# Kernel tuning notes

Hardware: AMD Instinct MI355X
Metric: run time of the kernel (lower is better)

## Reference

```python
import jax, jax.numpy as jnp
import numpy as np

D_MODEL = 1024
N_HEADS = 16
FACTOR = 2
KEY_DIM = D_MODEL // N_HEADS            # 64
HEAD_DIM = D_MODEL * FACTOR // N_HEADS  # 128
SCALING = KEY_DIM ** -0.5
BSZ, SEQ = 2, 2048


def _rel_pos(slen):
    # angle: 1/10000**linspace(0,1,key_dim//2), each value repeated twice
    half = jnp.asarray(1.0) / jnp.power(10000.0, jnp.linspace(0.0, 1.0, KEY_DIM // 2))
    angle = jnp.repeat(half, 2)                              # [key_dim]
    decay = jnp.log(1.0 - 2.0 ** (-5.0 - jnp.arange(N_HEADS, dtype=jnp.float32)))  # [h], negative
    idx = jnp.arange(slen, dtype=jnp.float32)
    sin = jnp.sin(idx[:, None] * angle[None, :])             # [s, key_dim]
    cos = jnp.cos(idx[:, None] * angle[None, :])
    diff = idx[:, None] - idx[None, :]                       # [s, s]
    tril = diff >= 0
    mask = jnp.where(tril[None], jnp.exp(diff[None] * decay[:, None, None]), 0.0)  # [h, s, s]
    mask = mask / jnp.sqrt(mask.sum(axis=-1, keepdims=True))
    return sin, cos, mask


def _rotate_every_two(x):
    x1 = x[..., ::2]
    x2 = x[..., 1::2]
    return jnp.stack((-x2, x1), axis=-1).reshape(x.shape)


def _theta_shift(x, sin, cos):
    return x * cos + _rotate_every_two(x) * sin


def setup_inputs() -> dict:
    key = jax.random.key(0)
    ks = jax.random.split(key, 11)
    s = 1.0 / np.sqrt(D_MODEL)
    s2 = 1.0 / np.sqrt(D_MODEL * FACTOR)
    return {
        "x": jax.random.normal(ks[0], (BSZ, SEQ, D_MODEL), jnp.float32),
        "q_w": jax.random.uniform(ks[1], (D_MODEL, D_MODEL), jnp.float32, -s, s),
        "q_b": jax.random.uniform(ks[2], (D_MODEL,), jnp.float32, -s, s),
        "k_w": jax.random.uniform(ks[3], (D_MODEL, D_MODEL), jnp.float32, -s, s),
        "k_b": jax.random.uniform(ks[4], (D_MODEL,), jnp.float32, -s, s),
        "v_w": jax.random.uniform(ks[5], (D_MODEL, D_MODEL * FACTOR), jnp.float32, -s, s),
        "v_b": jax.random.uniform(ks[6], (D_MODEL * FACTOR,), jnp.float32, -s, s),
        "g_w": jax.random.uniform(ks[7], (D_MODEL, D_MODEL * FACTOR), jnp.float32, -s, s),
        "g_b": jax.random.uniform(ks[8], (D_MODEL * FACTOR,), jnp.float32, -s, s),
        "o_w": jax.random.uniform(ks[9], (D_MODEL * FACTOR, D_MODEL), jnp.float32, -s2, s2),
        "o_b": jax.random.uniform(ks[10], (D_MODEL,), jnp.float32, -s2, s2),
    }


def _forward(x, q_w, q_b, k_w, k_b, v_w, v_b, g_w, g_b, o_w, o_b):
    bsz, slen, _ = x.shape
    sin, cos, mask = _rel_pos(slen)
    q = x @ q_w + q_b
    k = (x @ k_w + k_b) * SCALING
    v = x @ v_w + v_b
    g = x @ g_w + g_b
    # [b, h, s, key_dim]
    q = q.reshape(bsz, slen, N_HEADS, KEY_DIM).transpose(0, 2, 1, 3)
    k = k.reshape(bsz, slen, N_HEADS, KEY_DIM).transpose(0, 2, 1, 3)
    qr = _theta_shift(q, sin, cos)
    kr = _theta_shift(k, sin, cos)
    vr = v.reshape(bsz, slen, N_HEADS, HEAD_DIM).transpose(0, 2, 1, 3)  # [b,h,s,head_dim]
    qk = jnp.einsum('bhmd,bhnd->bhmn', qr, kr) * mask                  # decay-masked scores
    denom = jnp.clip(jnp.abs(jax.lax.stop_gradient(qk).sum(axis=-1, keepdims=True)), 1.0, None)
    qk = qk / denom
    out = jnp.einsum('bhmn,bhnd->bhmd', qk, vr).transpose(0, 2, 1, 3)  # [b,s,h,head_dim]
    # per-head LayerNorm over head_dim, no affine
    mu = out.mean(axis=-1, keepdims=True)
    var = out.var(axis=-1, keepdims=True)
    out = (out - mu) / jnp.sqrt(var + 1e-5)
    out = out.reshape(bsz, slen, N_HEADS * HEAD_DIM)
    out = jax.nn.silu(g) * out
    return out @ o_w + o_b


def reference(x, q_w, q_b, k_w, k_b, v_w, v_b, g_w, g_b, o_w, o_b):
    return _forward(x, q_w, q_b, k_w, k_b, v_w, v_b, g_w, g_b, o_w, o_b)
```

## Files before the change

kernel.cpp:

```cpp
#include <hip/hip_runtime.h>
#include <hip/hip_bf16.h>


typedef __hip_bfloat16 bf16;
typedef short bf16x4 __attribute__((ext_vector_type(4)));
typedef short bf16x8 __attribute__((ext_vector_type(8)));
typedef float floatx4 __attribute__((ext_vector_type(4)));

#define B_SZ 2
#define SEQ 2048
#define NH 16
#define KD 64
#define HD 128

#define ASYNC16(gp, lp)                                                             \
  __builtin_amdgcn_global_load_lds(                                                 \
      (const __attribute__((address_space(1))) unsigned int*)(unsigned long long)(const void*)(gp), \
      (__attribute__((address_space(3))) unsigned int*)(unsigned int)(unsigned long long)(void*)(lp), \
      16, 0, 0)

__device__ __forceinline__ float b2f(bf16 x) { return __bfloat162float(x); }
__device__ __forceinline__ bf16 f2b(float x) { return __float2bfloat16(x); }

__global__ void convert_k(const float* __restrict__ in, bf16* __restrict__ out) {
  int i = blockIdx.x * 256 + threadIdx.x;
  float4 v = reinterpret_cast<const float4*>(in)[i];
  union { bf16 h[4]; bf16x4 v4; } u;
  u.h[0] = f2b(v.x); u.h[1] = f2b(v.y); u.h[2] = f2b(v.z); u.h[3] = f2b(v.w);
  reinterpret_cast<bf16x4*>(out)[i] = u.v4;
}

__global__ void transpose_k(const float* __restrict__ in, bf16* __restrict__ out,
                            int K, int N) {
  __shared__ float tile[32][33];
  int tx = threadIdx.x, ty = threadIdx.y;
  int n0 = blockIdx.x * 32, k0 = blockIdx.y * 32;
#pragma unroll
  for (int j = 0; j < 4; ++j)
    tile[ty + j * 8][tx] = in[(size_t)(k0 + ty + j * 8) * N + n0 + tx];
  __syncthreads();
#pragma unroll
  for (int j = 0; j < 4; ++j)
    out[(size_t)(n0 + ty + j * 8) * K + k0 + tx] = f2b(tile[tx][ty + j * 8]);
}

__global__ void vtrans_k(const bf16* __restrict__ in, bf16* __restrict__ out) {
  __shared__ bf16 tile[32][34];
  int tx = threadIdx.x, ty = threadIdx.y;
  int s0 = blockIdx.x * 32, c0 = blockIdx.y * 32;
  const bf16* src = in + (size_t)blockIdx.z * 2048 * 2048;
  bf16* dst = out + (size_t)blockIdx.z * 2048 * 2048;
#pragma unroll
  for (int j = 0; j < 4; ++j)
    tile[ty + j * 8][tx] = src[(size_t)(s0 + ty + j * 8) * 2048 + c0 + tx];
  __syncthreads();
#pragma unroll
  for (int j = 0; j < 4; ++j)
    dst[(size_t)(c0 + ty + j * 8) * 2048 + s0 + tx] = tile[tx][ty + j * 8];
}

template <int BM, int BN, int KDIM, int MODE>
__global__ __launch_bounds__(256, 2) void gemm_bt(
    const bf16* __restrict__ A, const bf16* __restrict__ Bt, int Ndim,
    const float* __restrict__ bias_q, const float* __restrict__ bias_k,
    const float* __restrict__ bias_v, const float* __restrict__ bias_g,
    float* __restrict__ outCqk, bf16* __restrict__ out_v,
    float* __restrict__ out_g, float* __restrict__ outF) {
  __shared__ bf16 As[BM * 32];
  __shared__ bf16 Bs[BN * 32];
  const int tid = threadIdx.x;
  const int wave = tid >> 6, lane = tid & 63;
  const int quad = lane >> 4, l16 = lane & 15;
  const int m0 = blockIdx.y * BM, n0 = blockIdx.x * BN;
  constexpr int FI = BM / 32;
  constexpr int FJ = BN / 32;
  const int wm = (wave >> 1) * (BM / 2), wn = (wave & 1) * (BN / 2);

  floatx4 acc[FI][FJ] = {};

  for (int k0 = 0; k0 < KDIM; k0 += 32) {
#pragma unroll
    for (int j = 0; j < BM / 64; ++j) {
      int cbase = (j * 4 + wave) * 64;
      int c = cbase + lane;
      const bf16* g = A + (size_t)(m0 + (c >> 2)) * KDIM + k0 + (c & 3) * 8;
      ASYNC16(g, &As[cbase * 8]);
    }
#pragma unroll
    for (int j = 0; j < BN / 64; ++j) {
      int cbase = (j * 4 + wave) * 64;
      int c = cbase + lane;
      const bf16* g = Bt + (size_t)(n0 + (c >> 2)) * KDIM + k0 + (c & 3) * 8;
      ASYNC16(g, &Bs[cbase * 8]);
    }
    __syncthreads();

    bf16x8 af[FI], bfr[FJ];
#pragma unroll
    for (int i = 0; i < FI; ++i)
      af[i] = *(const bf16x8*)&As[(wm + i * 16 + l16) * 32 + quad * 8];
#pragma unroll
    for (int j = 0; j < FJ; ++j)
      bfr[j] = *(const bf16x8*)&Bs[(wn + j * 16 + l16) * 32 + quad * 8];
#pragma unroll
    for (int i = 0; i < FI; ++i)
#pragma unroll
      for (int j = 0; j < FJ; ++j)
        acc[i][j] = __builtin_amdgcn_mfma_f32_16x16x32_bf16(af[i], bfr[j],
                                                            acc[i][j], 0, 0, 0);
    __syncthreads();
  }

#pragma unroll
  for (int i = 0; i < FI; ++i) {
#pragma unroll
    for (int j = 0; j < FJ; ++j) {
#pragma unroll
      for (int r = 0; r < 4; ++r) {
        int gm = m0 + wm + i * 16 + quad * 4 + r;
        int gn = n0 + wn + j * 16 + l16;
        float v = acc[i][j][r];
        if (MODE == 1) {
          v += bias_q[gn];
          outF[(size_t)gm * Ndim + gn] = v;
        } else {
          if (gn < 2048) {
            bool is_k = gn >= 1024;
            int jj = is_k ? gn - 1024 : gn;
            v += is_k ? bias_k[jj] : bias_q[jj];
            if (is_k) v *= 0.125f;
            outCqk[(size_t)gm * 2048 + gn] = v;
          } else if (gn < 4096) {
            int jj = gn - 2048;
            v += bias_v[jj];
            out_v[(size_t)gm * 2048 + jj] = f2b(v);
          } else {
            int jj = gn - 4096;
            v += bias_g[jj];
            out_g[(size_t)gm * 2048 + jj] = v;
          }
        }
      }
    }
  }
}

__global__ void router_k(const float* __restrict__ Cqk,
                         bf16* __restrict__ qh, bf16* __restrict__ ql,
                         bf16* __restrict__ kh, bf16* __restrict__ kl) {
  int t = blockIdx.x * 256 + threadIdx.x;
  int row = t >> 10, pc = t & 1023;
  int b = row >> 11, s = row & 2047;
  bool is_k = pc >= 512;
  int jj = (pc - (is_k ? 512 : 0)) * 2;
  int h = jj >> 6, d = jj & 63, ii = d >> 1;
  float2 v = *(const float2*)&Cqk[(size_t)row * 2048 + pc * 2];
  float half = exp2f(-(float)ii * (13.287712379549449f / 31.0f));
  float ang = (float)s * half;
  float sn = sinf(ang), cs = cosf(ang);
  float e = v.x * cs - v.y * sn;
  float o = v.y * cs + v.x * sn;
  bf16 eh = f2b(e), oh = f2b(o);
  bf16 el = f2b(e - b2f(eh)), ol = f2b(o - b2f(oh));
  size_t idx = (((size_t)b * NH + h) * SEQ + s) * KD + d;
  bf16* ph = is_k ? kh : qh;
  bf16* pl = is_k ? kl : ql;
  union { bf16 h2[2]; unsigned u; } uh, ul;
  uh.h2[0] = eh; uh.h2[1] = oh;
  ul.h2[0] = el; ul.h2[1] = ol;
  *(unsigned*)&ph[idx] = uh.u;
  *(unsigned*)&pl[idx] = ul.u;
}

__global__ __launch_bounds__(128, 2) void retention_k(
    const bf16* __restrict__ qh, const bf16* __restrict__ ql,
    const bf16* __restrict__ kh, const bf16* __restrict__ kl,
    const bf16* __restrict__ vT, const float* __restrict__ g,
    bf16* __restrict__ gated) {
  __shared__ bf16 KHs[2][32 * 64];
  __shared__ bf16 KLs[2][32 * 64];
  __shared__ bf16 Vs[2][128 * 32];
  const int tid = threadIdx.x;
  const int wave = tid >> 6, lane = tid & 63;
  const int quad = lane >> 4, l16 = lane & 15;
  const int bid = blockIdx.x;
  const int px_raw = bid & 31;
  const int seg = bid >> 5;
  const int h = seg & 15, b = seg >> 4;
  const int px = ((seg >> 3) & 1) ? (31 - px_raw) : px_raw;
  const int bh = b * NH + h;
  const int bt_h = 63 - px;
  const int bt_l = px;
  const int m0h = bt_h * 32 + wave * 16;
  const int m0l = bt_l * 32 + wave * 16;
  const int ntiles = bt_h + 1;
  const int lt_ntiles = bt_l + 1;

  const float t = exp2f(-(float)(5 + h));
  const float lng = log1pf(-t);
  const float log2g = lng * 1.44269504088896340736f;

  float rfh, rfl;
  {
    int mh = m0h + l16, ml = m0l + l16;
    rfh = exp2f((float)mh * log2g) *
          rsqrtf(-expm1f((float)(mh + 1) * lng) / t);
    rfl = exp2f((float)ml * log2g) *
          rsqrtf(-expm1f((float)(ml + 1) * lng) / t);
  }
  const float gstep = exp2f(-32.0f * log2g);
  float cfq[8];
#pragma unroll
  for (int i = 0; i < 8; ++i) {
    int hh = i >> 2, r = i & 3;
    cfq[i] = exp2f(-(float)(hh * 16 + quad * 4 + r) * log2g);
  }

  const size_t qoffh = ((size_t)bh * SEQ + m0h + l16) * KD;
  const size_t qoffl = ((size_t)bh * SEQ + m0l + l16) * KD;
  bf16x8 aq0h_h = *(const bf16x8*)&qh[qoffh + quad * 8];
  bf16x8 aq1h_h = *(const bf16x8*)&qh[qoffh + 32 + quad * 8];
  bf16x8 aq0l_h = *(const bf16x8*)&ql[qoffh + quad * 8];
  bf16x8 aq1l_h = *(const bf16x8*)&ql[qoffh + 32 + quad * 8];
  bf16x8 aq0h_l = *(const bf16x8*)&qh[qoffl + quad * 8];
  bf16x8 aq1h_l = *(const bf16x8*)&qh[qoffl + 32 + quad * 8];
  bf16x8 aq0l_l = *(const bf16x8*)&ql[qoffl + quad * 8];
  bf16x8 aq1l_l = *(const bf16x8*)&ql[qoffl + 32 + quad * 8];

  floatx4 oacch[8] = {}, oaccl[8] = {};
  float rsh = 0.f, rsl = 0.f;

  const bf16* khb = kh + (size_t)bh * SEQ * KD;
  const bf16* klb = kl + (size_t)bh * SEQ * KD;
  const bf16* vbase = vT + (size_t)bh * HD * SEQ;

  auto stage = [&](int nt, int buf) {
    const int n0s = nt * 32;
#pragma unroll
    for (int j = 0; j < 8; ++j) {
      int cc = wave * 8 + j;
      if (cc < 8) {
        const bf16* src = (cc < 4) ? khb : klb;
        bf16* dst = (cc < 4) ? KHs[buf] : KLs[buf];
        int r = ((cc & 3) * 8) + (lane >> 3);
        int s = lane & 7;
        int q = (s - r) & 7;
        ASYNC16(src + (size_t)(n0s + r) * KD + q * 8, &dst[(cc & 3) * 512]);
      } else {
        int r = (cc - 8) * 16 + (lane >> 2);
        int s = lane & 3;
        int q = (s - (r >> 1)) & 3;
        ASYNC16(vbase + (size_t)r * SEQ + n0s + q * 8, &Vs[buf][(cc - 8) * 512]);
      }
    }
  };

  auto buildPA = [&](const floatx4* sc, float rf, float& rs, int n0,
                     int m0) -> bf16x8 {
    const int m = m0 + l16;
    const bool full = (m0 >= n0 + 31);
    unsigned d[4];
#pragma unroll
    for (int hh = 0; hh < 2; ++hh) {
      float p[4];
#pragma unroll
      for (int r = 0; r < 4; ++r) {
        float pv;
        if (full) {
          pv = sc[hh][r] * rf * cfq[hh * 4 + r];
        } else {
          int n = n0 + hh * 16 + quad * 4 + r;
          pv = (m >= n) ? sc[hh][r] * rf * cfq[hh * 4 + r] : 0.f;
        }
        rs += pv;
        p[r] = pv;
      }
      union { bf16 hx[2]; unsigned u; } u0, u1;
      u0.hx[0] = f2b(p[0]); u0.hx[1] = f2b(p[1]);
      u1.hx[0] = f2b(p[2]); u1.hx[1] = f2b(p[3]);
      d[hh * 2 + 0] = u0.u;
      d[hh * 2 + 1] = u1.u;
    }
    unsigned a0 = d[0], b0 = d[2];
    asm("v_permlane32_swap_b32 %0, %1" : "+v"(a0), "+v"(b0));
    asm("v_permlane16_swap_b32 %0, %1" : "+v"(a0), "+v"(b0));
    unsigned a1 = d[1], b1 = d[3];
    asm("v_permlane32_swap_b32 %0, %1" : "+v"(a1), "+v"(b1));
    asm("v_permlane16_swap_b32 %0, %1" : "+v"(a1), "+v"(b1));
    union { unsigned u[4]; bf16x8 v; } pu;
    pu.u[0] = a0; pu.u[1] = a1; pu.u[2] = b0; pu.u[3] = b1;
    return pu.v;
  };

  stage(0, 0);
  for (int nt = 0; nt < ntiles; ++nt) {
    const int n0 = nt * 32;
    const int cur = nt & 1;
    asm volatile("s_waitcnt vmcnt(0) lgkmcnt(0)" ::: "memory");
    __syncthreads();
    {
      int pf = (nt + 1 < ntiles) ? nt + 1 : nt;
      stage(pf, cur ^ 1);
    }

    const bool hact = (n0 <= m0h + 15);
    const bool lact = (n0 <= m0l + 15);

    floatx4 sch[2], scl[2];
#pragma unroll
    for (int hh = 0; hh < 2; ++hh) {
      int krow = hh * 16 + l16;
      int c0 = ((quad + krow) & 7) * 8;
      int c1 = ((quad + 4 + krow) & 7) * 8;
      bf16x8 bkh0 = *(const bf16x8*)&KHs[cur][krow * 64 + c0];
      bf16x8 bkh1 = *(const bf16x8*)&KHs[cur][krow * 64 + c1];
      bf16x8 bkl0 = *(const bf16x8*)&KLs[cur][krow * 64 + c0];
      bf16x8 bkl1 = *(const bf16x8*)&KLs[cur][krow * 64 + c1];
      if (hact) {
        floatx4 z1 = {0.f, 0.f, 0.f, 0.f}, z2 = z1, z3 = z1;
        z1 = __builtin_amdgcn_mfma_f32_16x16x32_bf16(bkh0, aq0h_h, z1, 0, 0, 0);
        z2 = __builtin_amdgcn_mfma_f32_16x16x32_bf16(bkh0, aq0l_h, z2, 0, 0, 0);
        z3 = __builtin_amdgcn_mfma_f32_16x16x32_bf16(bkl0, aq0h_h, z3, 0, 0, 0);
        z1 = __builtin_amdgcn_mfma_f32_16x16x32_bf16(bkh1, aq1h_h, z1, 0, 0, 0);
        z2 = __builtin_amdgcn_mfma_f32_16x16x32_bf16(bkh1, aq1l_h, z2, 0, 0, 0);
        z3 = __builtin_amdgcn_mfma_f32_16x16x32_bf16(bkl1, aq1h_h, z3, 0, 0, 0);
        sch[0 + hh] = z1 + z2 + z3;
      }
      if (lact) {
        floatx4 z1 = {0.f, 0.f, 0.f, 0.f}, z2 = z1, z3 = z1;
        z1 = __builtin_amdgcn_mfma_f32_16x16x32_bf16(bkh0, aq0h_l, z1, 0, 0, 0);
        z2 = __builtin_amdgcn_mfma_f32_16x16x32_bf16(bkh0, aq0l_l, z2, 0, 0, 0);
        z3 = __builtin_amdgcn_mfma_f32_16x16x32_bf16(bkl0, aq0h_l, z3, 0, 0, 0);
        z1 = __builtin_amdgcn_mfma_f32_16x16x32_bf16(bkh1, aq1h_l, z1, 0, 0, 0);
        z2 = __builtin_amdgcn_mfma_f32_16x16x32_bf16(bkh1, aq1l_l, z2, 0, 0, 0);
        z3 = __builtin_amdgcn_mfma_f32_16x16x32_bf16(bkl1, aq1h_l, z3, 0, 0, 0);
        scl[0 + hh] = z1 + z2 + z3;
      }
    }

    bf16x8 pah, pal;
    if (hact) pah = buildPA(sch, rfh, rsh, n0, m0h);
    if (lact) pal = buildPA(scl, rfl, rsl, n0, m0l);
    rfh *= gstep;
    if (nt + 1 < lt_ntiles) rfl *= gstep;

#pragma unroll
    for (int dt = 0; dt < 8; ++dt) {
      int vrow = dt * 16 + l16;
      bf16x8 bv = *(const bf16x8*)&Vs[cur][vrow * 32 + ((quad + (vrow >> 1)) & 3) * 8];
      if (hact)
        oacch[dt] = __builtin_amdgcn_mfma_f32_16x16x32_bf16(pah, bv, oacch[dt], 0, 0, 0);
      if (lact)
        oaccl[dt] = __builtin_amdgcn_mfma_f32_16x16x32_bf16(pal, bv, oaccl[dt], 0, 0, 0);
    }
  }

  auto finalize = [&](floatx4* oacc, float rowsum, int m0) {
    float v = rowsum;
    v += __shfl_xor(v, 16);
    v += __shfl_xor(v, 32);
    float inv_den[4];
#pragma unroll
    for (int r = 0; r < 4; ++r) {
      float dsum = __shfl(v, quad * 4 + r);
      inv_den[r] = 1.0f / fmaxf(fabsf(dsum), 1.0f);
    }
    float s1[4] = {}, s2[4] = {};
#pragma unroll
    for (int dt = 0; dt < 8; ++dt) {
#pragma unroll
      for (int r = 0; r < 4; ++r) {
        float vv = oacc[dt][r] * inv_den[r];
        oacc[dt][r] = vv;
        s1[r] += vv;
        s2[r] += vv * vv;
      }
    }
    float mean[4], istd[4];
#pragma unroll
    for (int r = 0; r < 4; ++r) {
      float a = s1[r], q2 = s2[r];
      a += __shfl_xor(a, 1); a += __shfl_xor(a, 2);
      a += __shfl_xor(a, 4); a += __shfl_xor(a, 8);
      q2 += __shfl_xor(q2, 1); q2 += __shfl_xor(q2, 2);
      q2 += __shfl_xor(q2, 4); q2 += __shfl_xor(q2, 8);
      mean[r] = a * (1.0f / 128.0f);
      float var = q2 * (1.0f / 128.0f) - mean[r] * mean[r];
      istd[r] = rsqrtf(fmaxf(var, 0.0f) + 1e-5f);
    }
#pragma unroll
    for (int dt = 0; dt < 8; ++dt) {
#pragma unroll
      for (int r = 0; r < 4; ++r) {
        int m = m0 + quad * 4 + r;
        int col = h * HD + dt * 16 + l16;
        float vv = (oacc[dt][r] - mean[r]) * istd[r];
        float gv = g[((size_t)b * SEQ + m) * 2048 + col];
        float sg = gv / (1.0f + expf(-gv));
        gated[((size_t)b * SEQ + m) * 2048 + col] = f2b(sg * vv);
      }
    }
  };
  finalize(oacch, rsh, m0h);
  finalize(oaccl, rsl, m0l);
}

extern "C" void kernel_launch(void* const* d_in, const int* in_sizes, int n_in,
                              void* d_out, int out_size, void* d_ws,
                              size_t ws_size, hipStream_t stream) {
  const float* x   = (const float*)d_in[0];
  const float* q_w = (const float*)d_in[1];
  const float* q_b = (const float*)d_in[2];
  const float* k_w = (const float*)d_in[3];
  const float* k_b = (const float*)d_in[4];
  const float* v_w = (const float*)d_in[5];
  const float* v_b = (const float*)d_in[6];
  const float* g_w = (const float*)d_in[7];
  const float* g_b = (const float*)d_in[8];
  const float* o_w = (const float*)d_in[9];
  const float* o_b = (const float*)d_in[10];

  char* ws = (char*)d_ws;
  bf16* Wt    = (bf16*)ws; ws += (size_t)6144 * 1024 * 2;
  bf16* oT    = (bf16*)ws; ws += (size_t)1024 * 2048 * 2;
  bf16* xb    = (bf16*)ws; ws += (size_t)4096 * 1024 * 2;
  float* Cqk  = (float*)ws; ws += (size_t)4096 * 2048 * 4;
  bf16* qhb   = (bf16*)ws; ws += (size_t)32 * 2048 * 64 * 2;
  bf16* qlb   = (bf16*)ws; ws += (size_t)32 * 2048 * 64 * 2;
  bf16* khb   = (bf16*)ws; ws += (size_t)32 * 2048 * 64 * 2;
  bf16* klb   = (bf16*)ws; ws += (size_t)32 * 2048 * 64 * 2;
  bf16* vTb   = (bf16*)ws; ws += (size_t)32 * 128 * 2048 * 2;
  float* gbuf = (float*)ws; ws += (size_t)2 * 2048 * 2048 * 4;
  bf16* gated = (bf16*)ws; ws += (size_t)4096 * 2048 * 2;
  bf16* vbuf  = gated;

  convert_k<<<(4096 * 1024 / 4) / 256, 256, 0, stream>>>(x, xb);

  dim3 tb(32, 8);
  transpose_k<<<dim3(1024 / 32, 1024 / 32), tb, 0, stream>>>(q_w, Wt, 1024, 1024);
  transpose_k<<<dim3(1024 / 32, 1024 / 32), tb, 0, stream>>>(k_w, Wt + (size_t)1024 * 1024, 1024, 1024);
  transpose_k<<<dim3(2048 / 32, 1024 / 32), tb, 0, stream>>>(v_w, Wt + (size_t)2048 * 1024, 1024, 2048);
  transpose_k<<<dim3(2048 / 32, 1024 / 32), tb, 0, stream>>>(g_w, Wt + (size_t)4096 * 1024, 1024, 2048);
  transpose_k<<<dim3(1024 / 32, 2048 / 32), tb, 0, stream>>>(o_w, oT, 2048, 1024);

  gemm_bt<128, 128, 1024, 0><<<dim3(6144 / 128, 4096 / 128), 256, 0, stream>>>(
      xb, Wt, 6144, q_b, k_b, v_b, g_b, Cqk, vbuf, gbuf, nullptr);

  vtrans_k<<<dim3(64, 64, B_SZ), tb, 0, stream>>>(vbuf, vTb);

  router_k<<<(4096 * 1024) / 256, 256, 0, stream>>>(Cqk, qhb, qlb, khb, klb);

  retention_k<<<dim3(1024), 128, 0, stream>>>(
      qhb, qlb, khb, klb, vTb, gbuf, gated);

  gemm_bt<128, 64, 2048, 1><<<dim3(1024 / 64, 4096 / 128), 256, 0, stream>>>(
      gated, oT, 1024, o_b, nullptr, nullptr, nullptr, nullptr, nullptr,
      nullptr, (float*)d_out);
}
```

Before: 352.4 us.

## Pre-swizzle V into MFMA fragment layout and load directly from global

```diff
diff --git a/kernel.cpp b/kernel.cpp
--- a/kernel.cpp
+++ b/kernel.cpp
@@ -21,6 +21,8 @@
 
 __device__ __forceinline__ float b2f(bf16 x) { return __bfloat162float(x); }
 __device__ __forceinline__ bf16 f2b(float x) { return __float2bfloat16(x); }
+
+#define MFMA16(a, bb, c) __builtin_amdgcn_mfma_f32_16x16x32_bf16(a, bb, c, 0, 0, 0)
 
 __global__ void convert_k(const float* __restrict__ in, bf16* __restrict__ out) {
   int i = blockIdx.x * 256 + threadIdx.x;
@@ -45,18 +47,28 @@
 }
 
 __global__ void vtrans_k(const bf16* __restrict__ in, bf16* __restrict__ out) {
-  __shared__ bf16 tile[32][34];
+  __shared__ bf16 tile[32][72];
   int tx = threadIdx.x, ty = threadIdx.y;
-  int s0 = blockIdx.x * 32, c0 = blockIdx.y * 32;
-  const bf16* src = in + (size_t)blockIdx.z * 2048 * 2048;
-  bf16* dst = out + (size_t)blockIdx.z * 2048 * 2048;
-#pragma unroll
-  for (int j = 0; j < 4; ++j)
-    tile[ty + j * 8][tx] = src[(size_t)(s0 + ty + j * 8) * 2048 + c0 + tx];
+  int s0 = blockIdx.x * 32, c0 = blockIdx.y * 64, bz = blockIdx.z;
+  const bf16* src = in + (size_t)bz * 2048 * 2048;
+#pragma unroll
+  for (int j = 0; j < 4; ++j) {
+    int sr = ty + j * 8;
+    tile[sr][tx] = src[(size_t)(s0 + sr) * 2048 + c0 + tx];
+    tile[sr][tx + 32] = src[(size_t)(s0 + sr) * 2048 + c0 + 32 + tx];
+  }
   __syncthreads();
-#pragma unroll
-  for (int j = 0; j < 4; ++j)
-    dst[(size_t)(c0 + ty + j * 8) * 2048 + s0 + tx] = tile[tx][ty + j * 8];
+  int tid = ty * 32 + tx;
+  int dl = tid & 63, srun = tid >> 6;
+  int c = c0 + dl, hh = c >> 7, d = c & 127;
+  int dt = d >> 4, lw = d & 15;
+  union { bf16 e[8]; bf16x8 v; } pk;
+#pragma unroll
+  for (int k = 0; k < 8; ++k) pk.e[k] = tile[srun * 8 + k][dl];
+  size_t bh = (size_t)bz * NH + hh;
+  int nt = s0 >> 5;
+  size_t idx = ((bh * 64 + nt) * 8 + dt) * 512 + (size_t)(srun * 16 + lw) * 8;
+  *(bf16x8*)&out[idx] = pk.v;
 }
 
 template <int BM, int BN, int KDIM, int MODE>
@@ -106,8 +118,7 @@
     for (int i = 0; i < FI; ++i)
 #pragma unroll
       for (int j = 0; j < FJ; ++j)
-        acc[i][j] = __builtin_amdgcn_mfma_f32_16x16x32_bf16(af[i], bfr[j],
-                                                            acc[i][j], 0, 0, 0);
+        acc[i][j] = MFMA16(af[i], bfr[j], acc[i][j]);
     __syncthreads();
   }
 
@@ -175,11 +186,10 @@
 __global__ __launch_bounds__(128, 2) void retention_k(
     const bf16* __restrict__ qh, const bf16* __restrict__ ql,
     const bf16* __restrict__ kh, const bf16* __restrict__ kl,
-    const bf16* __restrict__ vT, const float* __restrict__ g,
+    const bf16* __restrict__ vf, const float* __restrict__ g,
     bf16* __restrict__ gated) {
   __shared__ bf16 KHs[2][32 * 64];
   __shared__ bf16 KLs[2][32 * 64];
-  __shared__ bf16 Vs[2][128 * 32];
   const int tid = threadIdx.x;
   const int wave = tid >> 6, lane = tid & 63;
   const int quad = lane >> 4, l16 = lane & 15;
@@ -232,26 +242,20 @@
 
   const bf16* khb = kh + (size_t)bh * SEQ * KD;
   const bf16* klb = kl + (size_t)bh * SEQ * KD;
-  const bf16* vbase = vT + (size_t)bh * HD * SEQ;
+  const bf16* vfb = vf + (size_t)bh * 64 * 8 * 512;
+  const int lo8 = lane * 8;
 
   auto stage = [&](int nt, int buf) {
     const int n0s = nt * 32;
 #pragma unroll
-    for (int j = 0; j < 8; ++j) {
-      int cc = wave * 8 + j;
-      if (cc < 8) {
-        const bf16* src = (cc < 4) ? khb : klb;
-        bf16* dst = (cc < 4) ? KHs[buf] : KLs[buf];
-        int r = ((cc & 3) * 8) + (lane >> 3);
-        int s = lane & 7;
-        int q = (s - r) & 7;
-        ASYNC16(src + (size_t)(n0s + r) * KD + q * 8, &dst[(cc & 3) * 512]);
-      } else {
-        int r = (cc - 8) * 16 + (lane >> 2);
-        int s = lane & 3;
-        int q = (s - (r >> 1)) & 3;
-        ASYNC16(vbase + (size_t)r * SEQ + n0s + q * 8, &Vs[buf][(cc - 8) * 512]);
-      }
+    for (int j = 0; j < 4; ++j) {
+      int cc = wave * 4 + j;
+      const bf16* src = (cc < 4) ? khb : klb;
+      bf16* dst = (cc < 4) ? KHs[buf] : KLs[buf];
+      int r = ((cc & 3) * 8) + (lane >> 3);
+      int s = lane & 7;
+      int q = (s - r) & 7;
+      ASYNC16(src + (size_t)(n0s + r) * KD + q * 8, &dst[(cc & 3) * 512]);
     }
   };
 
@@ -298,6 +302,12 @@
     const int cur = nt & 1;
     asm volatile("s_waitcnt vmcnt(0) lgkmcnt(0)" ::: "memory");
     __syncthreads();
+
+    bf16x8 vv[8];
+#pragma unroll
+    for (int c = 0; c < 8; ++c)
+      vv[c] = *(const bf16x8*)(vfb + ((size_t)nt * 8 + c) * 512 + lo8);
+
     {
       int pf = (nt + 1 < ntiles) ? nt + 1 : nt;
       stage(pf, cur ^ 1);
@@ -318,23 +328,23 @@
       bf16x8 bkl1 = *(const bf16x8*)&KLs[cur][krow * 64 + c1];
       if (hact) {
         floatx4 z1 = {0.f, 0.f, 0.f, 0.f}, z2 = z1, z3 = z1;
-        z1 = __builtin_amdgcn_mfma_f32_16x16x32_bf16(bkh0, aq0h_h, z1, 0, 0, 0);
-        z2 = __builtin_amdgcn_mfma_f32_16x16x32_bf16(bkh0, aq0l_h, z2, 0, 0, 0);
-        z3 = __builtin_amdgcn_mfma_f32_16x16x32_bf16(bkl0, aq0h_h, z3, 0, 0, 0);
-        z1 = __builtin_amdgcn_mfma_f32_16x16x32_bf16(bkh1, aq1h_h, z1, 0, 0, 0);
-        z2 = __builtin_amdgcn_mfma_f32_16x16x32_bf16(bkh1, aq1l_h, z2, 0, 0, 0);
-        z3 = __builtin_amdgcn_mfma_f32_16x16x32_bf16(bkl1, aq1h_h, z3, 0, 0, 0);
-        sch[0 + hh] = z1 + z2 + z3;
+        z1 = MFMA16(bkh0, aq0h_h, z1);
+        z2 = MFMA16(bkh0, aq0l_h, z2);
+        z3 = MFMA16(bkl0, aq0h_h, z3);
+        z1 = MFMA16(bkh1, aq1h_h, z1);
+        z2 = MFMA16(bkh1, aq1l_h, z2);
+        z3 = MFMA16(bkl1, aq1h_h, z3);
+        sch[hh] = z1 + z2 + z3;
       }
       if (lact) {
         floatx4 z1 = {0.f, 0.f, 0.f, 0.f}, z2 = z1, z3 = z1;
-        z1 = __builtin_amdgcn_mfma_f32_16x16x32_bf16(bkh0, aq0h_l, z1, 0, 0, 0);
-        z2 = __builtin_amdgcn_mfma_f32_16x16x32_bf16(bkh0, aq0l_l, z2, 0, 0, 0);
-        z3 = __builtin_amdgcn_mfma_f32_16x16x32_bf16(bkl0, aq0h_l, z3, 0, 0, 0);
-        z1 = __builtin_amdgcn_mfma_f32_16x16x32_bf16(bkh1, aq1h_l, z1, 0, 0, 0);
-        z2 = __builtin_amdgcn_mfma_f32_16x16x32_bf16(bkh1, aq1l_l, z2, 0, 0, 0);
-        z3 = __builtin_amdgcn_mfma_f32_16x16x32_bf16(bkl1, aq1h_l, z3, 0, 0, 0);
-        scl[0 + hh] = z1 + z2 + z3;
+        z1 = MFMA16(bkh0, aq0h_l, z1);
+        z2 = MFMA16(bkh0, aq0l_l, z2);
+        z3 = MFMA16(bkl0, aq0h_l, z3);
+        z1 = MFMA16(bkh1, aq1h_l, z1);
+        z2 = MFMA16(bkh1, aq1l_l, z2);
+        z3 = MFMA16(bkl1, aq1h_l, z3);
+        scl[hh] = z1 + z2 + z3;
       }
     }
 
@@ -346,12 +356,8 @@
 
 #pragma unroll
     for (int dt = 0; dt < 8; ++dt) {
-      int vrow = dt * 16 + l16;
-      bf16x8 bv = *(const bf16x8*)&Vs[cur][vrow * 32 + ((quad + (vrow >> 1)) & 3) * 8];
-      if (hact)
-        oacch[dt] = __builtin_amdgcn_mfma_f32_16x16x32_bf16(pah, bv, oacch[dt], 0, 0, 0);
-      if (lact)
-        oaccl[dt] = __builtin_amdgcn_mfma_f32_16x16x32_bf16(pal, bv, oaccl[dt], 0, 0, 0);
+      if (hact) oacch[dt] = MFMA16(pah, vv[dt], oacch[dt]);
+      if (lact) oaccl[dt] = MFMA16(pal, vv[dt], oaccl[dt]);
     }
   }
 
@@ -370,10 +376,10 @@
     for (int dt = 0; dt < 8; ++dt) {
 #pragma unroll
       for (int r = 0; r < 4; ++r) {
-        float vv = oacc[dt][r] * inv_den[r];
-        oacc[dt][r] = vv;
-        s1[r] += vv;
-        s2[r] += vv * vv;
+        float vv2 = oacc[dt][r] * inv_den[r];
+        oacc[dt][r] = vv2;
+        s1[r] += vv2;
+        s2[r] += vv2 * vv2;
       }
     }
     float mean[4], istd[4];
@@ -394,10 +400,10 @@
       for (int r = 0; r < 4; ++r) {
         int m = m0 + quad * 4 + r;
         int col = h * HD + dt * 16 + l16;
-        float vv = (oacc[dt][r] - mean[r]) * istd[r];
+        float vv2 = (oacc[dt][r] - mean[r]) * istd[r];
         float gv = g[((size_t)b * SEQ + m) * 2048 + col];
         float sg = gv / (1.0f + expf(-gv));
-        gated[((size_t)b * SEQ + m) * 2048 + col] = f2b(sg * vv);
+        gated[((size_t)b * SEQ + m) * 2048 + col] = f2b(sg * vv2);
       }
     }
   };
@@ -429,7 +435,7 @@
   bf16* qlb   = (bf16*)ws; ws += (size_t)32 * 2048 * 64 * 2;
   bf16* khb   = (bf16*)ws; ws += (size_t)32 * 2048 * 64 * 2;
   bf16* klb   = (bf16*)ws; ws += (size_t)32 * 2048 * 64 * 2;
-  bf16* vTb   = (bf16*)ws; ws += (size_t)32 * 128 * 2048 * 2;
+  bf16* vfb   = (bf16*)ws; ws += (size_t)32 * 64 * 8 * 512 * 2;
   float* gbuf = (float*)ws; ws += (size_t)2 * 2048 * 2048 * 4;
   bf16* gated = (bf16*)ws; ws += (size_t)4096 * 2048 * 2;
   bf16* vbuf  = gated;
@@ -446,12 +452,12 @@
   gemm_bt<128, 128, 1024, 0><<<dim3(6144 / 128, 4096 / 128), 256, 0, stream>>>(
       xb, Wt, 6144, q_b, k_b, v_b, g_b, Cqk, vbuf, gbuf, nullptr);
 
-  vtrans_k<<<dim3(64, 64, B_SZ), tb, 0, stream>>>(vbuf, vTb);
+  vtrans_k<<<dim3(2048 / 32, 2048 / 64, B_SZ), tb, 0, stream>>>(vbuf, vfb);
 
   router_k<<<(4096 * 1024) / 256, 256, 0, stream>>>(Cqk, qhb, qlb, khb, klb);
 
   retention_k<<<dim3(1024), 128, 0, stream>>>(
-      qhb, qlb, khb, klb, vTb, gbuf, gated);
+      qhb, qlb, khb, klb, vfb, gbuf, gated);
 
   gemm_bt<128, 64, 2048, 1><<<dim3(1024 / 64, 4096 / 128), 256, 0, stream>>>(
       gated, oT, 1024, o_b, nullptr, nullptr, nullptr, nullptr, nullptr,
```

Measured after the change: 341.3 us. -3.1%, faster.
